# Performance work log

Hardware: AMD Instinct MI355X
Metric: run time of the kernel (lower is better)

## Reference

```python
import jax, jax.numpy as jnp
from jax import lax
import numpy as np

B = 512       # number of sequences
L = 512       # max_seq_length
A = 20        # amino-acid alphabet / input_size
C = 8         # conv channels
N_REST = 8    # total_layers - 1 extra conv+pool blocks (log2(512)=9)
STD = 0.01    # non-trainable self.std


def setup_inputs() -> dict:
    key = jax.random.key(0)
    k1, k2, k3, k4 = jax.random.split(key, 4)
    # one-hot residue encoding, as the nonzero()-based scatters assume
    aa = jax.random.randint(k1, (B, L), 0, A)
    x = jax.nn.one_hot(aa, A, dtype=jnp.float32)          # (B, L, 20)
    masks = jnp.ones((B, L), dtype=jnp.float32)           # unused by forward
    # BLOSUM-like integer substitution matrix
    blosum = jax.random.randint(k2, (A, A), -4, 12).astype(jnp.float32)
    blosum = (blosum + blosum.T) / 2.0
    lpm = blosum                                          # trainable copy
    pm = jnp.clip(blosum, 0.0, None)                      # clamped buffer
    w_first = jax.random.normal(k3, (C, 1, 3), dtype=jnp.float32) * 0.3
    w_rest = jax.random.normal(k4, (N_REST, C, C, 3), dtype=jnp.float32) * 0.2
    return {"x": x, "masks": masks, "lpm": lpm, "pm": pm,
            "w_first": w_first, "w_rest": w_rest}


def _column(xp, lpm, pm):
    # xp: (B, 20, L). For each nonzero (b,i,p), the torch loops write
    # value(i->k) at (b,k,p): k=i+1..18 uses lpm[i,k]*pm[i,k];
    # k=0..i-1 uses lpm[k,i]*pm[k,i]; column k=19 and diag never written.
    nz = (xp != 0).astype(xp.dtype)
    prod = jnp.clip(lpm, 1e-3, 1.0) * pm                  # (20,20)
    i = jnp.arange(A)[:, None]
    k = jnp.arange(A)[None, :]
    V = jnp.where(k > i, prod, jnp.where(k < i, prod.T, 0.0))
    V = V.at[:, A - 1].set(0.0)                           # k=19 never written
    return jnp.einsum('bip,ik->bkp', nz, V)


def _row(xp):
    # Gaussian-decay neighbor writes at p +/- d (d=1,2,3), indices clamped
    # to [0, L-1]; later (larger-d) index_put calls overwrite earlier ones.
    nz = (xp != 0).astype(xp.dtype)
    ar = jnp.arange(L)
    new_x = jnp.zeros_like(xp)
    for d in (1, 2, 3):
        val = jnp.exp(jnp.asarray(-(d * d) / (2.0 * STD * STD), xp.dtype))
        up = jnp.zeros_like(nz).at[:, :, jnp.clip(ar + d, 0, L - 1)].max(nz)
        dn = jnp.zeros_like(nz).at[:, :, jnp.clip(ar - d, 0, L - 1)].max(nz)
        new_x = jnp.where(jnp.maximum(up, dn) > 0, val, new_x)
    return new_x


def _convs(h, w_first, w_rest):
    dn = ('NCH', 'OIH', 'NCH')
    h = lax.conv_general_dilated(h, w_first, (1,), ((1, 1),),
                                 dimension_numbers=dn)
    h = h.reshape(h.shape[0], h.shape[1], -1, 2).mean(-1)   # AvgPool1d(2)
    for li in range(N_REST):
        h = lax.conv_general_dilated(h, w_rest[li], (1,), ((1, 1),),
                                     dimension_numbers=dn)
        h = h.reshape(h.shape[0], h.shape[1], -1, 2).mean(-1)
    return h  # (N, C, 1)


def reference(x, masks, lpm, pm, w_first, w_rest):
    seq_num = x.shape[0]
    xp = jnp.transpose(x, (0, 2, 1))                        # (B, 20, L)
    xp = xp + _column(xp, lpm, pm) + _row(xp)
    h = xp.reshape(seq_num * A, 1, L)
    h = _convs(h, w_first, w_rest)                          # (B*20, 8, 1)
    return h.squeeze(-1).reshape(seq_num, A, -1)            # (B, 20, 8)
```

## Files before the change

kernel.cpp:

```cpp
#include <hip/hip_runtime.h>


__global__ __launch_bounds__(64) void build_Weff(
        const float* __restrict__ wf,
        const float* __restrict__ wr,
        float* __restrict__ Weff){
    int p = blockIdx.x, t = threadIdx.x;
    int c = t >> 3, u = t & 7;
    __shared__ float winA[64];
    __shared__ float winB[64];
    __shared__ float taps[256];

    int base = (p >> 1) - 1; if (base < 0) base = 0;
    {
        float w0 = wf[c*3+0], w1 = wf[c*3+1], w2 = wf[c*3+2];
        float tap0 = 0.5f*w0, tap1 = 0.5f*(w0+w1), tap2 = 0.5f*(w1+w2), tap3 = 0.5f*w2;
        int q = base + u;
        float v = 0.f;
        if (q < 256){
            int j = p - 2*q;
            if (j == -1) v = tap0;
            else if (j == 0) v = tap1;
            else if (j == 1) v = tap2;
            else if (j == 2) v = tap3;
        }
        winA[c*8+u] = v;
    }
    float* inw  = winA;
    float* outw = winB;
    int Ln = 256;
    for (int l = 0; l < 8; l++){
        {
            const float* w = wr + ((l*8 + c)*8 + u)*3;
            float w0 = w[0], w1 = w[1], w2 = w[2];
            taps[t*4+0] = 0.5f*w0;
            taps[t*4+1] = 0.5f*(w0+w1);
            taps[t*4+2] = 0.5f*(w1+w2);
            taps[t*4+3] = 0.5f*w2;
        }
        __syncthreads();
        int Lo = Ln >> 1;
        int nb = (base - 2) >> 1; if (nb < 0) nb = 0;
        int q = nb + u;
        float acc = 0.f;
        if (q < Lo){
            #pragma unroll
            for (int ci = 0; ci < 8; ci++){
                const float* tp = &taps[(c*8+ci)*4];
                #pragma unroll
                for (int j = -1; j <= 2; j++){
                    int m  = 2*q + j;
                    int wi = m - base;
                    float h = (m >= 0 && m < Ln && wi >= 0 && wi < 8)
                              ? inw[ci*8 + wi] : 0.f;
                    acc += tp[j+1] * h;
                }
            }
        }
        outw[c*8+u] = acc;
        float* tmp = inw; inw = outw; outw = tmp;
        base = nb; Ln = Lo;
        __syncthreads();
    }
    if (u == 0) Weff[c*512 + p] = inw[c*8 + 0];
}

__global__ __launch_bounds__(256) void cnn_main(
        const float* __restrict__ x,
        const float* __restrict__ Weff,
        const float* __restrict__ lpm,
        const float* __restrict__ pm,
        float* __restrict__ out){
    int b = blockIdx.x, t = threadIdx.x;
    __shared__ float W[4096];
    __shared__ float T[4][160];
    __shared__ float Ts[160];
    for (int idx = t; idx < 4096; idx += 256) W[idx] = Weff[idx];
    for (int idx = t; idx < 640; idx += 256) (&T[0][0])[idx] = 0.f;
    __syncthreads();
    const float* xb = x + (size_t)b * 10240;
    int wid = t >> 6;
    for (int p = t; p < 512; p += 256){
        const float4* f4 = (const float4*)(xb + p*20);
        int aa = 0;
        #pragma unroll
        for (int j = 0; j < 5; j++){
            float4 v = f4[j];
            if (v.x != 0.f) aa = 4*j + 0;
            if (v.y != 0.f) aa = 4*j + 1;
            if (v.z != 0.f) aa = 4*j + 2;
            if (v.w != 0.f) aa = 4*j + 3;
        }
        #pragma unroll
        for (int c = 0; c < 8; c++)
            atomicAdd(&T[wid][c*20 + aa], W[c*512 + p]);
    }
    __syncthreads();
    if (t < 160) Ts[t] = T[0][t] + T[1][t] + T[2][t] + T[3][t];
    __syncthreads();
    if (t < 160){
        int k = t >> 3, c = t & 7;
        float acc = Ts[c*20 + k];
        if (k != 19){
            #pragma unroll
            for (int i = 0; i < 20; i++){
                if (i == k) continue;
                int r  = (i < k) ? i : k;
                int cc = (i < k) ? k : i;
                float l = fminf(fmaxf(lpm[r*20 + cc], 1e-3f), 1.0f);
                acc += Ts[c*20 + i] * (l * pm[r*20 + cc]);
            }
        }
        out[(size_t)b*160 + t] = acc;
    }
}

extern "C" void kernel_launch(void* const* d_in, const int* in_sizes, int n_in,
                              void* d_out, int out_size, void* d_ws, size_t ws_size,
                              hipStream_t stream){
    const float* x   = (const float*)d_in[0];
    const float* lpm = (const float*)d_in[2];
    const float* pm  = (const float*)d_in[3];
    const float* wf  = (const float*)d_in[4];
    const float* wr  = (const float*)d_in[5];
    float* Weff = (float*)d_ws;

    hipLaunchKernelGGL(build_Weff, dim3(512), dim3(64),  0, stream, wf, wr, Weff);
    hipLaunchKernelGGL(cnn_main,   dim3(512), dim3(256), 0, stream, x, Weff, lpm, pm,
                       (float*)d_out);
}
```

Measured before the change: 98.16 us.

## Prefetch conv weights, widen main kernel to 512 threads, precompute substitution matrix

```diff
diff --git a/kernel.cpp b/kernel.cpp
--- a/kernel.cpp
+++ b/kernel.cpp
@@ -10,6 +10,13 @@
     __shared__ float winA[64];
     __shared__ float winB[64];
     __shared__ float taps[256];
+
+    float tw0[8], tw1[8], tw2[8];
+    #pragma unroll
+    for (int l = 0; l < 8; l++){
+        const float* w = wr + ((l*8 + c)*8 + u)*3;
+        tw0[l] = w[0]; tw1[l] = w[1]; tw2[l] = w[2];
+    }
 
     int base = (p >> 1) - 1; if (base < 0) base = 0;
     {
@@ -31,8 +38,7 @@
     int Ln = 256;
     for (int l = 0; l < 8; l++){
         {
-            const float* w = wr + ((l*8 + c)*8 + u)*3;
-            float w0 = w[0], w1 = w[1], w2 = w[2];
+            float w0 = tw0[l], w1 = tw1[l], w2 = tw2[l];
             taps[t*4+0] = 0.5f*w0;
             taps[t*4+1] = 0.5f*(w0+w1);
             taps[t*4+2] = 0.5f*(w1+w2);
@@ -65,7 +71,7 @@
     if (u == 0) Weff[c*512 + p] = inw[c*8 + 0];
 }
 
-__global__ __launch_bounds__(256) void cnn_main(
+__global__ __launch_bounds__(512) void cnn_main(
         const float* __restrict__ x,
         const float* __restrict__ Weff,
         const float* __restrict__ lpm,
@@ -73,14 +79,29 @@
         float* __restrict__ out){
     int b = blockIdx.x, t = threadIdx.x;
     __shared__ float W[4096];
-    __shared__ float T[4][160];
+    __shared__ float V[400];
+    __shared__ float T[8][160];
     __shared__ float Ts[160];
-    for (int idx = t; idx < 4096; idx += 256) W[idx] = Weff[idx];
-    for (int idx = t; idx < 640; idx += 256) (&T[0][0])[idx] = 0.f;
+    for (int idx = t; idx < 1024; idx += 512)
+        ((float4*)W)[idx] = ((const float4*)Weff)[idx];
+    if (t < 400){
+        int i = t / 20, k = t % 20;
+        float v = 0.f;
+        if (k != 19 && k != i){
+            int r  = (k > i) ? i : k;
+            int cc = (k > i) ? k : i;
+            float l = fminf(fmaxf(lpm[r*20 + cc], 1e-3f), 1.0f);
+            v = l * pm[r*20 + cc];
+        }
+        V[t] = v;
+    }
+    for (int idx = t; idx < 1280; idx += 512) (&T[0][0])[idx] = 0.f;
     __syncthreads();
+
     const float* xb = x + (size_t)b * 10240;
     int wid = t >> 6;
-    for (int p = t; p < 512; p += 256){
+    {
+        int p = t;
         const float4* f4 = (const float4*)(xb + p*20);
         int aa = 0;
         #pragma unroll
@@ -96,21 +117,19 @@
             atomicAdd(&T[wid][c*20 + aa], W[c*512 + p]);
     }
     __syncthreads();
-    if (t < 160) Ts[t] = T[0][t] + T[1][t] + T[2][t] + T[3][t];
+    if (t < 160){
+        float s = 0.f;
+        #pragma unroll
+        for (int w = 0; w < 8; w++) s += T[w][t];
+        Ts[t] = s;
+    }
     __syncthreads();
     if (t < 160){
         int k = t >> 3, c = t & 7;
         float acc = Ts[c*20 + k];
-        if (k != 19){
-            #pragma unroll
-            for (int i = 0; i < 20; i++){
-                if (i == k) continue;
-                int r  = (i < k) ? i : k;
-                int cc = (i < k) ? k : i;
-                float l = fminf(fmaxf(lpm[r*20 + cc], 1e-3f), 1.0f);
-                acc += Ts[c*20 + i] * (l * pm[r*20 + cc]);
-            }
-        }
+        #pragma unroll
+        for (int i = 0; i < 20; i++)
+            acc += Ts[c*20 + i] * V[i*20 + k];
         out[(size_t)b*160 + t] = acc;
     }
 }
@@ -126,6 +145,6 @@
     float* Weff = (float*)d_ws;
 
     hipLaunchKernelGGL(build_Weff, dim3(512), dim3(64),  0, stream, wf, wr, Weff);
-    hipLaunchKernelGGL(cnn_main,   dim3(512), dim3(256), 0, stream, x, Weff, lpm, pm,
+    hipLaunchKernelGGL(cnn_main,   dim3(512), dim3(512), 0, stream, x, Weff, lpm, pm,
                        (float*)d_out);
 }
```

Measured after the change: 91.49 us. -6.8%, faster.
